# Optimization experiments

Measured on AMD Instinct MI355X. Metric: run time of the kernel, lower is better.

Reference implementation:

```python
import jax, jax.numpy as jnp
import numpy as np

N_NODES = 100000
N_EDGES = 1600000
D_NODE = 32
D_EDGE = 16
D_HID = 64
D_OUT = 32


def setup_inputs() -> dict:
    key = jax.random.key(0)
    ks = jax.random.split(key, 7)
    x = jax.random.normal(ks[0], (N_NODES, D_NODE), dtype=jnp.float32)
    edge_index = jax.random.randint(ks[1], (2, N_EDGES), 0, N_NODES, dtype=jnp.int64)
    edge_attr = jax.random.normal(ks[2], (N_EDGES, D_EDGE), dtype=jnp.float32)
    # 2-layer MLP params (Linear -> ReLU -> Linear), He-ish scaling
    W1 = jax.random.normal(ks[3], (D_NODE + D_EDGE, D_HID), dtype=jnp.float32) * (2.0 / (D_NODE + D_EDGE)) ** 0.5
    b1 = jnp.zeros((D_HID,), dtype=jnp.float32)
    W2 = jax.random.normal(ks[4], (D_HID, D_OUT), dtype=jnp.float32) * (2.0 / D_HID) ** 0.5
    b2 = jnp.zeros((D_OUT,), dtype=jnp.float32)
    return {"x": x, "edge_index": edge_index, "edge_attr": edge_attr,
            "W1": W1, "b1": b1, "W2": W2, "b2": b2}


def reference(x, edge_index, edge_attr, W1, b1, W2, b2):
    row, col = edge_index[0], edge_index[1]
    # gather source-node feats and concat with edge feats: [E, d_node + d_edge]
    inp = jnp.concatenate([x[col], edge_attr], axis=1)
    # 2-layer MLP over edges
    h = jax.nn.relu(inp @ W1 + b1)
    messages = h @ W2 + b2  # [E, d_out]
    # scatter-sum aggregate by destination node
    message = jax.ops.segment_sum(messages, row, num_segments=x.shape[0])
    return message
```

## Files before the change

### kernel.cpp

```cpp
#include <hip/hip_runtime.h>
#include <hip/hip_bf16.h>
#include <stdint.h>

#define N_NODES 100000
#define N_EDGES 1600000
#define D_NODE  32
#define D_EDGE  16
#define D_IN    48
#define D_HID   64
#define D_OUT   32

#define NFLAGS_OFF  ((size_t)0)
#define NB1_OFF     ((size_t)64)
#define NB2_OFF     ((size_t)320)
#define W1BF_OFF    ((size_t)1024)
#define W2BF_OFF    ((size_t)9216)
#define COUNTS_OFF  ((size_t)65536)
#define OFFSETS_OFF ((size_t)466944)
#define BLKSUM_OFF  ((size_t)917504)
#define RANK_OFF    ((size_t)1048576)
#define MSG_OFF     ((size_t)8388608)

#define SCAN_NB 391

typedef __attribute__((ext_vector_type(8))) short bf16x8;
typedef __attribute__((ext_vector_type(4))) float f32x4;

__device__ inline float bf2f(unsigned int u16) {
    return __uint_as_float(u16 << 16);
}
__device__ inline unsigned short f2bf_rne(float f) {
    unsigned int x = __float_as_uint(f);
    unsigned int r = (x + 0x7FFFu + ((x >> 16) & 1u)) >> 16;
    return (unsigned short)r;
}
__device__ inline unsigned int pk_bf2(float a, float b) {
    float2 f; f.x = a; f.y = b;
    __hip_bfloat162 h = __float22bfloat162_rn(f);
    return *reinterpret_cast<unsigned int*>(&h);
}
__device__ inline float ld_f(const void* p, int i, int isbf) {
    if (isbf) return bf2f(((const unsigned short*)p)[i]);
    return ((const float*)p)[i];
}
__device__ inline bf16x8 pack_bf8(float4 v0, float4 v1) {
    union { unsigned int u[4]; bf16x8 v; } r;
    r.u[0] = pk_bf2(v0.x, v0.y);
    r.u[1] = pk_bf2(v0.z, v0.w);
    r.u[2] = pk_bf2(v1.x, v1.y);
    r.u[3] = pk_bf2(v1.z, v1.w);
    return r.v;
}

__global__ __launch_bounds__(256) void prep_kernel(
        const void* __restrict__ xq, const void* __restrict__ idxq,
        const void* __restrict__ W1q, const void* __restrict__ b1q,
        const void* __restrict__ W2q, const void* __restrict__ b2q,
        char* __restrict__ ws) {
    const int t = threadIdx.x;
    const int i0 = blockIdx.x * 256 + t;
    int* counts = (int*)(ws + COUNTS_OFF);
    if (i0 < N_NODES) counts[i0] = 0;
    if (blockIdx.x != 0) return;

    __shared__ int s_isbf;
    if (t < 64) {
        unsigned short u = ((const unsigned short*)xq)[t];
        unsigned long long mb = __ballot(((u >> 7) & 0xFF) >= 140);
        int wodd = ((const int*)idxq)[2 * t + 1];
        unsigned long long mi = __ballot(wodd != 0);
        if (t == 0) {
            int* flags = (int*)(ws + NFLAGS_OFF);
            flags[0] = (mb == 0ULL);
            flags[1] = (mi == 0ULL);
            s_isbf = (mb == 0ULL);
        }
    }
    __syncthreads();
    const int isbf = s_isbf;
    float* b1 = (float*)(ws + NB1_OFF);
    float* b2 = (float*)(ws + NB2_OFF);
    unsigned short* w1b = (unsigned short*)(ws + W1BF_OFF);
    unsigned short* w2b = (unsigned short*)(ws + W2BF_OFF);

    if (t < D_HID) b1[t] = ld_f(b1q, t, isbf);
    if (t < D_OUT) b2[t] = ld_f(b2q, t, isbf);

    for (int i = t; i < D_HID * 64; i += 256) {
        int n = i >> 6, k = i & 63;
        float v = (k < D_IN) ? ld_f(W1q, k * D_HID + n, isbf) : 0.0f;
        w1b[i] = f2bf_rne(v);
    }
    for (int i = t; i < D_OUT * 64; i += 256) {
        int n = i >> 6, k = i & 63;
        w2b[i] = f2bf_rne(ld_f(W2q, k * D_OUT + n, isbf));
    }
}

__global__ __launch_bounds__(256) void hist_kernel(const void* __restrict__ idxq,
                                                   char* __restrict__ ws,
                                                   int* __restrict__ rankb) {
    const int is64 = ((const int*)(ws + NFLAGS_OFF))[1];
    const int e = blockIdx.x * 256 + threadIdx.x;
    int dst;
    if (is64) dst = (int)((const long long*)idxq)[e];
    else      dst = ((const int*)idxq)[e];
    rankb[e] = atomicAdd((int*)(ws + COUNTS_OFF) + dst, 1);
}

__global__ __launch_bounds__(256) void scan_block_kernel(char* __restrict__ ws) {
    __shared__ int s[256];
    const int* counts = (const int*)(ws + COUNTS_OFF);
    int* offs   = (int*)(ws + OFFSETS_OFF);
    int* blksum = (int*)(ws + BLKSUM_OFF);
    const int t = threadIdx.x;
    const int i = blockIdx.x * 256 + t;
    int v = (i < N_NODES) ? counts[i] : 0;
    s[t] = v;
    __syncthreads();
    for (int d = 1; d < 256; d <<= 1) {
        int a = (t >= d) ? s[t - d] : 0;
        __syncthreads();
        s[t] += a;
        __syncthreads();
    }
    if (i < N_NODES) offs[i] = s[t] - v;
    if (t == 255) blksum[blockIdx.x] = s[255];
}

__global__ __launch_bounds__(256) void scan_add_kernel(char* __restrict__ ws) {
    __shared__ int s[256];
    int* offs = (int*)(ws + OFFSETS_OFF);
    const int* blksum = (const int*)(ws + BLKSUM_OFF);
    const int t = threadIdx.x;
    const int b = blockIdx.x;
    int acc = 0;
    for (int j = t; j < b; j += 256) acc += blksum[j];
    s[t] = acc;
    __syncthreads();
    for (int d = 128; d > 0; d >>= 1) {
        if (t < d) s[t] += s[t + d];
        __syncthreads();
    }
    const int prefix = s[0];
    const int i = b * 256 + t;
    if (i < N_NODES) offs[i] += prefix;
    if (i == 0) offs[N_NODES] = N_EDGES;
}

__global__ __launch_bounds__(256) void edge_mlp_mfma_kernel(
        const void* __restrict__ xq,
        const void* __restrict__ idxq,
        const void* __restrict__ eaq,
        const char* __restrict__ wsro,
        const int* __restrict__ rankb,
        unsigned short* __restrict__ msg) {
    const int isbf = ((const int*)(wsro + NFLAGS_OFF))[0];
    const int is64 = ((const int*)(wsro + NFLAGS_OFF))[1];

    __shared__ __align__(16) unsigned short hbuf[4][2][16][72];

    const int w   = threadIdx.x >> 6;
    const int l   = threadIdx.x & 63;
    const int m16 = l & 15;
    const int q   = l >> 4;

    const unsigned short* w1b = (const unsigned short*)(wsro + W1BF_OFF);
    const unsigned short* w2b = (const unsigned short*)(wsro + W2BF_OFF);
    const float* b1 = (const float*)(wsro + NB1_OFF);
    const float* b2 = (const float*)(wsro + NB2_OFF);
    const int* offs = (const int*)(wsro + OFFSETS_OFF);

    bf16x8 w1f[4][2], w2f[2][2];
#pragma unroll
    for (int t = 0; t < 4; ++t)
#pragma unroll
        for (int c = 0; c < 2; ++c)
            w1f[t][c] = *(const bf16x8*)(w1b + ((t * 16 + m16) * 64 + c * 32 + q * 8));
#pragma unroll
    for (int t = 0; t < 2; ++t)
#pragma unroll
        for (int c = 0; c < 2; ++c)
            w2f[t][c] = *(const bf16x8*)(w2b + ((t * 16 + m16) * 64 + c * 32 + q * 8));

    const int eb = blockIdx.x * 256 + w * 64;

    int srcv[4], posv[4];
#pragma unroll
    for (int g = 0; g < 4; ++g) {
        const int e = eb + g * 16 + m16;
        int dst;
        if (is64) {
            const long long* ip = (const long long*)idxq;
            dst = (int)ip[e];
            srcv[g] = (int)ip[N_EDGES + e];
        } else {
            const int* ip = (const int*)idxq;
            dst = ip[e];
            srcv[g] = ip[N_EDGES + e];
        }
        posv[g] = offs[dst] + rankb[e];
    }

    bf16x8 A0[4], A1[4];
#pragma unroll
    for (int g = 0; g < 4; ++g) {
        const int e = eb + g * 16 + m16;
        if (isbf) {
            const unsigned short* x  = (const unsigned short*)xq;
            const unsigned short* ea = (const unsigned short*)eaq;
            A0[g] = *(const bf16x8*)(x + (size_t)srcv[g] * D_NODE + q * 8);
            A1[g] = *(const bf16x8*)(ea + (size_t)e * D_EDGE + (q & 1) * 8);
        } else {
            const float* x  = (const float*)xq;
            const float* ea = (const float*)eaq;
            const float4* xp = (const float4*)(x + (size_t)srcv[g] * D_NODE + q * 8);
            A0[g] = pack_bf8(xp[0], xp[1]);
            const float4* ap = (const float4*)(ea + (size_t)e * D_EDGE + (q & 1) * 8);
            A1[g] = pack_bf8(ap[0], ap[1]);
        }
    }

    const float b1v[4] = { b1[m16], b1[16 + m16], b1[32 + m16], b1[48 + m16] };
    const float b2v[2] = { b2[m16], b2[16 + m16] };
    const int mrow = l >> 2;
    const int sub  = l & 3;

    auto L1 = [&](int g, int b) {
#pragma unroll
        for (int t = 0; t < 4; ++t) {
            f32x4 c;
            c[0] = c[1] = c[2] = c[3] = b1v[t];
            c = __builtin_amdgcn_mfma_f32_16x16x32_bf16(A0[g], w1f[t][0], c, 0, 0, 0);
            c = __builtin_amdgcn_mfma_f32_16x16x32_bf16(A1[g], w1f[t][1], c, 0, 0, 0);
            unsigned int u0 = pk_bf2(fmaxf(c[0], 0.0f), fmaxf(c[1], 0.0f));
            unsigned int u1 = pk_bf2(fmaxf(c[2], 0.0f), fmaxf(c[3], 0.0f));
            hbuf[w][b][q * 4 + 0][t * 16 + m16] = (unsigned short)u0;
            hbuf[w][b][q * 4 + 1][t * 16 + m16] = (unsigned short)(u0 >> 16);
            hbuf[w][b][q * 4 + 2][t * 16 + m16] = (unsigned short)u1;
            hbuf[w][b][q * 4 + 3][t * 16 + m16] = (unsigned short)(u1 >> 16);
        }
    };
    auto L2S = [&](int g, int b) {
        bf16x8 a20 = *(const bf16x8*)(&hbuf[w][b][m16][q * 8]);
        bf16x8 a21 = *(const bf16x8*)(&hbuf[w][b][m16][32 + q * 8]);
#pragma unroll
        for (int t = 0; t < 2; ++t) {
            f32x4 c;
            c[0] = c[1] = c[2] = c[3] = b2v[t];
            c = __builtin_amdgcn_mfma_f32_16x16x32_bf16(a20, w2f[t][0], c, 0, 0, 0);
            c = __builtin_amdgcn_mfma_f32_16x16x32_bf16(a21, w2f[t][1], c, 0, 0, 0);
            unsigned int u0 = pk_bf2(c[0], c[1]);
            unsigned int u1 = pk_bf2(c[2], c[3]);
            hbuf[w][b][q * 4 + 0][t * 16 + m16] = (unsigned short)u0;
            hbuf[w][b][q * 4 + 1][t * 16 + m16] = (unsigned short)(u0 >> 16);
            hbuf[w][b][q * 4 + 2][t * 16 + m16] = (unsigned short)u1;
            hbuf[w][b][q * 4 + 3][t * 16 + m16] = (unsigned short)(u1 >> 16);
        }
        const int posm = __shfl(posv[g], mrow, 64);
        uint4 rowv = *(const uint4*)(&hbuf[w][b][mrow][sub * 8]);
        *(uint4*)(msg + (size_t)posm * D_OUT + sub * 8) = rowv;
    };

    L1(0, 0);
    L1(1, 1);
    L2S(0, 0);
    L1(2, 0);
    L2S(1, 1);
    L1(3, 1);
    L2S(2, 0);
    L2S(3, 1);
}

__global__ __launch_bounds__(256) void reduce_kernel(
        const char* __restrict__ wsro, const unsigned short* __restrict__ msg,
        void* __restrict__ out) {
    const int isbf = ((const int*)(wsro + NFLAGS_OFF))[0];
    const int* offs = (const int*)(wsro + OFFSETS_OFF);
    const int t = blockIdx.x * 256 + threadIdx.x;
    const int node = t >> 4;
    if (node >= N_NODES) return;
    const int c2 = t & 15;
    const int lo = offs[node], hi = offs[node + 1];
    float s0 = 0.0f, s1 = 0.0f;
    const unsigned int* p = (const unsigned int*)msg + (size_t)lo * 16 + c2;
    int k = lo;
    for (; k + 1 < hi; k += 2) {
        unsigned int a = p[0], b = p[16];
        s0 += __uint_as_float(a << 16) + __uint_as_float(b << 16);
        s1 += __uint_as_float(a & 0xFFFF0000u) + __uint_as_float(b & 0xFFFF0000u);
        p += 32;
    }
    if (k < hi) {
        unsigned int a = p[0];
        s0 += __uint_as_float(a << 16);
        s1 += __uint_as_float(a & 0xFFFF0000u);
    }
    if (isbf) {
        ((unsigned int*)out)[(size_t)node * 16 + c2] = pk_bf2(s0, s1);
    } else {
        float2 v; v.x = s0; v.y = s1;
        ((float2*)out)[(size_t)node * 16 + c2] = v;
    }
}

extern "C" void kernel_launch(void* const* d_in, const int* in_sizes, int n_in,
                              void* d_out, int out_size, void* d_ws, size_t ws_size,
                              hipStream_t stream) {
    const void* x   = d_in[0];
    const void* idx = d_in[1];
    const void* ea  = d_in[2];
    const void* W1  = d_in[3];
    const void* b1  = d_in[4];
    const void* W2  = d_in[5];
    const void* b2  = d_in[6];
    char* ws = (char*)d_ws;

    hipLaunchKernelGGL(prep_kernel, dim3(SCAN_NB), dim3(256), 0, stream,
                       x, idx, W1, b1, W2, b2, ws);

    hipLaunchKernelGGL(hist_kernel, dim3(N_EDGES / 256), dim3(256), 0, stream,
                       idx, ws, (int*)(ws + RANK_OFF));

    hipLaunchKernelGGL(scan_block_kernel, dim3(SCAN_NB), dim3(256), 0, stream, ws);
    hipLaunchKernelGGL(scan_add_kernel,   dim3(SCAN_NB), dim3(256), 0, stream, ws);

    hipLaunchKernelGGL(edge_mlp_mfma_kernel, dim3(N_EDGES / 256), dim3(256), 0, stream,
                       x, idx, ea, (const char*)ws,
                       (const int*)(ws + RANK_OFF), (unsigned short*)(ws + MSG_OFF));

    hipLaunchKernelGGL(reduce_kernel, dim3((N_NODES * 16 + 255) / 256), dim3(256), 0, stream,
                       (const char*)ws, (const unsigned short*)(ws + MSG_OFF), d_out);
}
```

Before: 373.9 us.

## Sort edges by destination first, then reduce segments in-wave with float atomics

Edges are now bucketed by destination before the MLP runs. A scatter pass writes packed (src, edge id, dst) records into a CSR-ordered buffer. The MLP kernel reads these sorted records, sums runs of identical destinations within each 16-row tile using ballot and shuffles, and atomically adds the partial sums into an fp32 accumulator. A small kernel then converts the accumulator to the output. This removes the bf16 message buffer write and the separate reduce pass, at the cost of an extra atomic scatter pass, random gathers of edge_attr by edge id, and float atomics with nondeterministic summation order.

```diff
diff --git a/kernel.cpp b/kernel.cpp
--- a/kernel.cpp
+++ b/kernel.cpp
@@ -17,11 +17,13 @@
 #define W2BF_OFF    ((size_t)9216)
 #define COUNTS_OFF  ((size_t)65536)
 #define OFFSETS_OFF ((size_t)466944)
-#define BLKSUM_OFF  ((size_t)917504)
-#define RANK_OFF    ((size_t)1048576)
-#define MSG_OFF     ((size_t)8388608)
+#define CURSOR_OFF  ((size_t)917504)
+#define BLKSUM_OFF  ((size_t)1376256)
+#define REC_OFF     ((size_t)2097152)
+#define ACCUM_OFF   ((size_t)16777216)
 
 #define SCAN_NB 391
+#define EDGE_NB (N_EDGES / 256)
 
 typedef __attribute__((ext_vector_type(8))) short bf16x8;
 typedef __attribute__((ext_vector_type(4))) float f32x4;
@@ -61,6 +63,11 @@
     const int i0 = blockIdx.x * 256 + t;
     int* counts = (int*)(ws + COUNTS_OFF);
     if (i0 < N_NODES) counts[i0] = 0;
+
+    float4* acc4 = (float4*)(ws + ACCUM_OFF);
+    float4 z; z.x = z.y = z.z = z.w = 0.0f;
+    for (int i = i0; i < N_NODES * 32 / 4; i += SCAN_NB * 256) acc4[i] = z;
+
     if (blockIdx.x != 0) return;
 
     __shared__ int s_isbf;
@@ -98,14 +105,13 @@
 }
 
 __global__ __launch_bounds__(256) void hist_kernel(const void* __restrict__ idxq,
-                                                   char* __restrict__ ws,
-                                                   int* __restrict__ rankb) {
+                                                   char* __restrict__ ws) {
     const int is64 = ((const int*)(ws + NFLAGS_OFF))[1];
     const int e = blockIdx.x * 256 + threadIdx.x;
     int dst;
     if (is64) dst = (int)((const long long*)idxq)[e];
     else      dst = ((const int*)idxq)[e];
-    rankb[e] = atomicAdd((int*)(ws + COUNTS_OFF) + dst, 1);
+    atomicAdd((int*)(ws + COUNTS_OFF) + dst, 1);
 }
 
 __global__ __launch_bounds__(256) void scan_block_kernel(char* __restrict__ ws) {
@@ -130,7 +136,8 @@
 
 __global__ __launch_bounds__(256) void scan_add_kernel(char* __restrict__ ws) {
     __shared__ int s[256];
-    int* offs = (int*)(ws + OFFSETS_OFF);
+    int* offs   = (int*)(ws + OFFSETS_OFF);
+    int* cursor = (int*)(ws + CURSOR_OFF);
     const int* blksum = (const int*)(ws + BLKSUM_OFF);
     const int t = threadIdx.x;
     const int b = blockIdx.x;
@@ -144,19 +151,41 @@
     }
     const int prefix = s[0];
     const int i = b * 256 + t;
-    if (i < N_NODES) offs[i] += prefix;
+    if (i < N_NODES) {
+        int v = offs[i] + prefix;
+        offs[i]   = v;
+        cursor[i] = v;
+    }
     if (i == 0) offs[N_NODES] = N_EDGES;
 }
 
-__global__ __launch_bounds__(256) void edge_mlp_mfma_kernel(
+__global__ __launch_bounds__(256) void scatter_kernel(const void* __restrict__ idxq,
+                                                      char* __restrict__ ws) {
+    const int is64 = ((const int*)(ws + NFLAGS_OFF))[1];
+    const int e = blockIdx.x * 256 + threadIdx.x;
+    int dst, src;
+    if (is64) {
+        const long long* ip = (const long long*)idxq;
+        dst = (int)ip[e];
+        src = (int)ip[N_EDGES + e];
+    } else {
+        const int* ip = (const int*)idxq;
+        dst = ip[e];
+        src = ip[N_EDGES + e];
+    }
+    int pos = atomicAdd((int*)(ws + CURSOR_OFF) + dst, 1);
+    unsigned long long r = (unsigned long long)(unsigned)src
+                         | ((unsigned long long)(unsigned)e   << 17)
+                         | ((unsigned long long)(unsigned)dst << 38);
+    ((unsigned long long*)(ws + REC_OFF))[pos] = r;
+}
+
+__global__ __launch_bounds__(256) void edge_mlp_agg_kernel(
         const void* __restrict__ xq,
-        const void* __restrict__ idxq,
         const void* __restrict__ eaq,
         const char* __restrict__ wsro,
-        const int* __restrict__ rankb,
-        unsigned short* __restrict__ msg) {
+        float* __restrict__ accum) {
     const int isbf = ((const int*)(wsro + NFLAGS_OFF))[0];
-    const int is64 = ((const int*)(wsro + NFLAGS_OFF))[1];
 
     __shared__ __align__(16) unsigned short hbuf[4][2][16][72];
 
@@ -169,7 +198,7 @@
     const unsigned short* w2b = (const unsigned short*)(wsro + W2BF_OFF);
     const float* b1 = (const float*)(wsro + NB1_OFF);
     const float* b2 = (const float*)(wsro + NB2_OFF);
-    const int* offs = (const int*)(wsro + OFFSETS_OFF);
+    const unsigned long long* rec = (const unsigned long long*)(wsro + REC_OFF);
 
     bf16x8 w1f[4][2], w2f[2][2];
 #pragma unroll
@@ -183,48 +212,37 @@
         for (int c = 0; c < 2; ++c)
             w2f[t][c] = *(const bf16x8*)(w2b + ((t * 16 + m16) * 64 + c * 32 + q * 8));
 
-    const int eb = blockIdx.x * 256 + w * 64;
-
-    int srcv[4], posv[4];
+    const int kb = blockIdx.x * 256 + w * 64;
+
+    int srcv[4], ev[4], dstv[4];
 #pragma unroll
     for (int g = 0; g < 4; ++g) {
-        const int e = eb + g * 16 + m16;
-        int dst;
-        if (is64) {
-            const long long* ip = (const long long*)idxq;
-            dst = (int)ip[e];
-            srcv[g] = (int)ip[N_EDGES + e];
-        } else {
-            const int* ip = (const int*)idxq;
-            dst = ip[e];
-            srcv[g] = ip[N_EDGES + e];
-        }
-        posv[g] = offs[dst] + rankb[e];
+        unsigned long long r = rec[kb + g * 16 + m16];
+        srcv[g] = (int)(r & 0x1FFFFULL);
+        ev[g]   = (int)((r >> 17) & 0x1FFFFFULL);
+        dstv[g] = (int)(r >> 38);
     }
 
     bf16x8 A0[4], A1[4];
 #pragma unroll
     for (int g = 0; g < 4; ++g) {
-        const int e = eb + g * 16 + m16;
         if (isbf) {
             const unsigned short* x  = (const unsigned short*)xq;
             const unsigned short* ea = (const unsigned short*)eaq;
             A0[g] = *(const bf16x8*)(x + (size_t)srcv[g] * D_NODE + q * 8);
-            A1[g] = *(const bf16x8*)(ea + (size_t)e * D_EDGE + (q & 1) * 8);
+            A1[g] = *(const bf16x8*)(ea + (size_t)ev[g] * D_EDGE + (q & 1) * 8);
         } else {
             const float* x  = (const float*)xq;
             const float* ea = (const float*)eaq;
             const float4* xp = (const float4*)(x + (size_t)srcv[g] * D_NODE + q * 8);
             A0[g] = pack_bf8(xp[0], xp[1]);
-            const float4* ap = (const float4*)(ea + (size_t)e * D_EDGE + (q & 1) * 8);
+            const float4* ap = (const float4*)(ea + (size_t)ev[g] * D_EDGE + (q & 1) * 8);
             A1[g] = pack_bf8(ap[0], ap[1]);
         }
     }
 
     const float b1v[4] = { b1[m16], b1[16 + m16], b1[32 + m16], b1[48 + m16] };
     const float b2v[2] = { b2[m16], b2[16 + m16] };
-    const int mrow = l >> 2;
-    const int sub  = l & 3;
 
     auto L1 = [&](int g, int b) {
 #pragma unroll
@@ -241,66 +259,69 @@
             hbuf[w][b][q * 4 + 3][t * 16 + m16] = (unsigned short)(u1 >> 16);
         }
     };
-    auto L2S = [&](int g, int b) {
+
+    auto L2R = [&](int g, int b) {
         bf16x8 a20 = *(const bf16x8*)(&hbuf[w][b][m16][q * 8]);
         bf16x8 a21 = *(const bf16x8*)(&hbuf[w][b][m16][32 + q * 8]);
-#pragma unroll
-        for (int t = 0; t < 2; ++t) {
-            f32x4 c;
-            c[0] = c[1] = c[2] = c[3] = b2v[t];
-            c = __builtin_amdgcn_mfma_f32_16x16x32_bf16(a20, w2f[t][0], c, 0, 0, 0);
-            c = __builtin_amdgcn_mfma_f32_16x16x32_bf16(a21, w2f[t][1], c, 0, 0, 0);
-            unsigned int u0 = pk_bf2(c[0], c[1]);
-            unsigned int u1 = pk_bf2(c[2], c[3]);
-            hbuf[w][b][q * 4 + 0][t * 16 + m16] = (unsigned short)u0;
-            hbuf[w][b][q * 4 + 1][t * 16 + m16] = (unsigned short)(u0 >> 16);
-            hbuf[w][b][q * 4 + 2][t * 16 + m16] = (unsigned short)u1;
-            hbuf[w][b][q * 4 + 3][t * 16 + m16] = (unsigned short)(u1 >> 16);
+        f32x4 c0, c1;
+        c0[0] = c0[1] = c0[2] = c0[3] = b2v[0];
+        c1[0] = c1[1] = c1[2] = c1[3] = b2v[1];
+        c0 = __builtin_amdgcn_mfma_f32_16x16x32_bf16(a20, w2f[0][0], c0, 0, 0, 0);
+        c0 = __builtin_amdgcn_mfma_f32_16x16x32_bf16(a21, w2f[0][1], c0, 0, 0, 0);
+        c1 = __builtin_amdgcn_mfma_f32_16x16x32_bf16(a20, w2f[1][0], c1, 0, 0, 0);
+        c1 = __builtin_amdgcn_mfma_f32_16x16x32_bf16(a21, w2f[1][1], c1, 0, 0, 0);
+
+        const int dstw = dstv[g];
+        int dprev = __shfl(dstw, (m16 + 15) & 15, 16);
+        bool isStart = (m16 == 0) || (dprev != dstw);
+        unsigned long long bal = __ballot(isStart);
+        unsigned mask16 = (unsigned)(bal >> (l & 48)) & 0xFFFFu;
+        int start = 0;
+        while (start < 16) {
+            unsigned rest = mask16 >> 1 >> start;
+            int next = rest ? (start + 1 + (int)__builtin_ctz(rest)) : 16;
+            int d = __shfl(dstw, start, 16);
+            float s0 = 0.0f, s1 = 0.0f;
+#pragma unroll
+            for (int r = 0; r < 4; ++r) {
+                int m = q * 4 + r;
+                bool in = (m >= start) && (m < next);
+                s0 += in ? c0[r] : 0.0f;
+                s1 += in ? c1[r] : 0.0f;
+            }
+            s0 += __shfl_xor(s0, 16); s0 += __shfl_xor(s0, 32);
+            s1 += __shfl_xor(s1, 16); s1 += __shfl_xor(s1, 32);
+            if (q == 0) {
+                unsafeAtomicAdd(accum + (size_t)d * 32 + m16,      s0);
+                unsafeAtomicAdd(accum + (size_t)d * 32 + 16 + m16, s1);
+            }
+            start = next;
         }
-        const int posm = __shfl(posv[g], mrow, 64);
-        uint4 rowv = *(const uint4*)(&hbuf[w][b][mrow][sub * 8]);
-        *(uint4*)(msg + (size_t)posm * D_OUT + sub * 8) = rowv;
     };
 
     L1(0, 0);
     L1(1, 1);
-    L2S(0, 0);
+    L2R(0, 0);
     L1(2, 0);
-    L2S(1, 1);
+    L2R(1, 1);
     L1(3, 1);
-    L2S(2, 0);
-    L2S(3, 1);
-}
-
-__global__ __launch_bounds__(256) void reduce_kernel(
-        const char* __restrict__ wsro, const unsigned short* __restrict__ msg,
+    L2R(2, 0);
+    L2R(3, 1);
+}
+
+__global__ __launch_bounds__(256) void convert_kernel(
+        const char* __restrict__ wsro, const float* __restrict__ accum,
         void* __restrict__ out) {
     const int isbf = ((const int*)(wsro + NFLAGS_OFF))[0];
-    const int* offs = (const int*)(wsro + OFFSETS_OFF);
-    const int t = blockIdx.x * 256 + threadIdx.x;
-    const int node = t >> 4;
-    if (node >= N_NODES) return;
-    const int c2 = t & 15;
-    const int lo = offs[node], hi = offs[node + 1];
-    float s0 = 0.0f, s1 = 0.0f;
-    const unsigned int* p = (const unsigned int*)msg + (size_t)lo * 16 + c2;
-    int k = lo;
-    for (; k + 1 < hi; k += 2) {
-        unsigned int a = p[0], b = p[16];
-        s0 += __uint_as_float(a << 16) + __uint_as_float(b << 16);
-        s1 += __uint_as_float(a & 0xFFFF0000u) + __uint_as_float(b & 0xFFFF0000u);
-        p += 32;
-    }
-    if (k < hi) {
-        unsigned int a = p[0];
-        s0 += __uint_as_float(a << 16);
-        s1 += __uint_as_float(a & 0xFFFF0000u);
-    }
+    const int i = blockIdx.x * 256 + threadIdx.x;
+    float4 v = ((const float4*)accum)[i];
     if (isbf) {
-        ((unsigned int*)out)[(size_t)node * 16 + c2] = pk_bf2(s0, s1);
+        uint2 u;
+        u.x = pk_bf2(v.x, v.y);
+        u.y = pk_bf2(v.z, v.w);
+        ((uint2*)out)[i] = u;
     } else {
-        float2 v; v.x = s0; v.y = s1;
-        ((float2*)out)[(size_t)node * 16 + c2] = v;
+        ((float4*)out)[i] = v;
     }
 }
 
@@ -319,16 +340,16 @@
     hipLaunchKernelGGL(prep_kernel, dim3(SCAN_NB), dim3(256), 0, stream,
                        x, idx, W1, b1, W2, b2, ws);
 
-    hipLaunchKernelGGL(hist_kernel, dim3(N_EDGES / 256), dim3(256), 0, stream,
-                       idx, ws, (int*)(ws + RANK_OFF));
+    hipLaunchKernelGGL(hist_kernel, dim3(EDGE_NB), dim3(256), 0, stream, idx, ws);
 
     hipLaunchKernelGGL(scan_block_kernel, dim3(SCAN_NB), dim3(256), 0, stream, ws);
     hipLaunchKernelGGL(scan_add_kernel,   dim3(SCAN_NB), dim3(256), 0, stream, ws);
 
-    hipLaunchKernelGGL(edge_mlp_mfma_kernel, dim3(N_EDGES / 256), dim3(256), 0, stream,
-                       x, idx, ea, (const char*)ws,
-                       (const int*)(ws + RANK_OFF), (unsigned short*)(ws + MSG_OFF));
-
-    hipLaunchKernelGGL(reduce_kernel, dim3((N_NODES * 16 + 255) / 256), dim3(256), 0, stream,
-                       (const char*)ws, (const unsigned short*)(ws + MSG_OFF), d_out);
-}
+    hipLaunchKernelGGL(scatter_kernel, dim3(EDGE_NB), dim3(256), 0, stream, idx, ws);
+
+    hipLaunchKernelGGL(edge_mlp_agg_kernel, dim3(EDGE_NB), dim3(256), 0, stream,
+                       x, ea, (const char*)ws, (float*)(ws + ACCUM_OFF));
+
+    hipLaunchKernelGGL(convert_kernel, dim3(N_NODES * 32 / 4 / 256), dim3(256), 0, stream,
+                       (const char*)ws, (const float*)(ws + ACCUM_OFF), d_out);
+}
```

After: 452.6 us. +21.0%, slower.
